# Kernel optimization log

Measured on AMD Instinct MI355X. Metric: run time of the kernel, lower is better.

## Reference

```python
import jax, jax.numpy as jnp
import numpy as np

N_HEAD = 16
D_HEAD = 64
MAX_REL = 512  # max_relative_positions


def setup_inputs() -> dict:
    key = jax.random.key(0)
    ks = jax.random.split(key, 9)
    B, S, D = 2, 2048, 1024
    return {
        "hidden_states": jax.random.normal(ks[0], (B, S, D), jnp.float32),
        "Wq": jax.random.normal(ks[1], (D, D), jnp.float32) * 0.02,
        "bq": jnp.zeros((D,), jnp.float32),
        "Wk": jax.random.normal(ks[2], (D, D), jnp.float32) * 0.02,
        "bk": jnp.zeros((D,), jnp.float32),
        "Wv": jax.random.normal(ks[3], (D, D), jnp.float32) * 0.02,
        "bv": jnp.zeros((D,), jnp.float32),
        "Wc": jax.random.normal(ks[4], (D, D), jnp.float32) * 0.02,
        "pos_table": jax.random.normal(ks[5], (2 * MAX_REL, D_HEAD), jnp.float32) * 0.02,
    }


def reference(hidden_states, Wq, bq, Wk, bk, Wv, bv, Wc, pos_table):
    B, S, D = hidden_states.shape
    H, Dh = N_HEAD, D_HEAD

    # QKV projections (torch Linear: x @ W.T + b)
    q = hidden_states @ Wq.T + bq
    k = hidden_states @ Wk.T + bk
    v = hidden_states @ Wv.T + bv
    q = q.reshape(B, S, H, Dh).transpose(0, 2, 1, 3)  # b h s d
    k = k.reshape(B, S, H, Dh).transpose(0, 2, 1, 3)
    v = v.reshape(B, S, H, Dh).transpose(0, 2, 1, 3)

    # relative position embedding lookup: [S, S, Dh]
    ar = jnp.arange(S)
    rel = jnp.clip(ar[:, None] - ar[None, :] + MAX_REL, 0, 2 * MAX_REL - 1)
    rpe = pos_table[rel]  # (S, S, Dh)

    # c2p: original einsum 'bhld,ijd->bhij' sums q over l (faithful)
    c2p = jnp.einsum('bhld,ijd->bhij', q, rpe)
    p2c = jnp.einsum('bhjd,ijd->bhij', k, jnp.flip(rpe, axis=0))
    bias = c2p + p2c  # (B, H, S, S)

    # SDPA with explicit attn_mask == bias added to scaled scores
    scale = 1.0 / jnp.sqrt(jnp.asarray(Dh, hidden_states.dtype))
    scores = jnp.einsum('bhid,bhjd->bhij', q, k) * scale + bias
    attn = jax.nn.softmax(scores, axis=-1)
    out = jnp.einsum('bhij,bhjd->bhid', attn, v)  # (B, H, S, Dh)

    out = out.transpose(0, 2, 1, 3).reshape(B, S, D)
    return out @ Wc.T  # c_proj has no bias; dropout is identity in eval
```

## Files before the change

### kernel.cpp

```cpp
#include <hip/hip_runtime.h>
#include <math.h>

#define BN   2
#define SEQ  2048
#define DIM  1024
#define NH   16
#define DH   64
#define TAB  1024
#define SCALE 0.125f
#define LOG2E 1.44269504088896340736f

typedef __attribute__((ext_vector_type(8))) short bf16x8;
typedef __attribute__((ext_vector_type(4))) float f32x4;

#if defined(__has_builtin)
#if __has_builtin(__builtin_amdgcn_exp2f)
#define EXP2F(x) __builtin_amdgcn_exp2f(x)
#else
#define EXP2F(x) exp2f(x)
#endif
#else
#define EXP2F(x) exp2f(x)
#endif

__device__ __forceinline__ short f2b(float f) {
    union { float f; unsigned u; } x; x.f = f;
    return (short)((x.u + 0x7fffu + ((x.u >> 16) & 1u)) >> 16);
}
__device__ __forceinline__ float b2f(short s) {
    union { float f; unsigned u; } x; x.u = ((unsigned)(unsigned short)s) << 16;
    return x.f;
}

#define GLDS16(gp, lp) __builtin_amdgcn_global_load_lds( \
    (const __attribute__((address_space(1))) void*)(gp), \
    (__attribute__((address_space(3))) void*)(lp), 16, 0, 0)

__device__ __forceinline__ bf16x8 fragS(const short* base, int row, int kq) {
    return *(const bf16x8*)(base + row * 64 + ((kq ^ (row & 7)) << 3));
}

__global__ __launch_bounds__(256) void f2b_multi_kernel(
    const float* __restrict__ s0, short* __restrict__ d0, int n0,
    const float* __restrict__ s1, short* __restrict__ d1,
    const float* __restrict__ s2, short* __restrict__ d2,
    const float* __restrict__ s3, short* __restrict__ d3, int nw,
    const float* __restrict__ s4, short* __restrict__ d4, int n4)
{
    const int z = blockIdx.z;
    const float* src = z == 0 ? s0 : (z == 1 ? s1 : (z == 2 ? s2 : (z == 3 ? s3 : s4)));
    short* dst       = z == 0 ? d0 : (z == 1 ? d1 : (z == 2 ? d2 : (z == 3 ? d3 : d4)));
    const int n      = z == 0 ? n0 : (z == 4 ? n4 : nw);
    int i = (blockIdx.x * 256 + threadIdx.x) * 8;
    if (i >= n) return;
    float4 a = *(const float4*)&src[i];
    float4 b = *(const float4*)&src[i + 4];
    bf16x8 o = { f2b(a.x), f2b(a.y), f2b(a.z), f2b(a.w),
                 f2b(b.x), f2b(b.y), f2b(b.z), f2b(b.w) };
    *(bf16x8*)&dst[i] = o;
}

__global__ __launch_bounds__(256) void qkv_mfma_kernel(
    const short* __restrict__ xb,
    const short* __restrict__ Wqb, const float* __restrict__ bq,
    const short* __restrict__ Wkb, const float* __restrict__ bk,
    const short* __restrict__ Wvb, const float* __restrict__ bv,
    short* __restrict__ q, short* __restrict__ k, short* __restrict__ v)
{
    const int which = blockIdx.z;
    const short* W    = which == 0 ? Wqb : (which == 1 ? Wkb : Wvb);
    const float* bias = which == 0 ? bq  : (which == 1 ? bk  : bv);
    short* outp       = which == 0 ? q   : (which == 1 ? k   : v);
    const float osc   = which == 0 ? SCALE * LOG2E : 1.0f;

    const int m0 = blockIdx.y * 128;
    const int n0 = blockIdx.x * 128;

    __shared__ short As[128 * 64];
    __shared__ short Bs[128 * 64];

    const int t  = threadIdx.x;
    const int w  = t >> 6;
    const int q4 = (t >> 4) & 3;
    const int l  = t & 15;
    const int wm = (w >> 1) * 64;
    const int wn = (w & 1) * 64;

    f32x4 acc[4][4];
#pragma unroll
    for (int mt = 0; mt < 4; ++mt)
#pragma unroll
        for (int nt = 0; nt < 4; ++nt) acc[mt][nt] = (f32x4){0.f,0.f,0.f,0.f};

    for (int k0 = 0; k0 < DIM; k0 += 64) {
        __syncthreads();
#pragma unroll
        for (int p = 0; p < 4; ++p) {
            const int cq = p * 256 + t;
            const int row = cq >> 3, bd = cq & 7;
            const int goff = (bd ^ (row & 7)) << 3;
            GLDS16(xb + (size_t)(m0 + row) * DIM + k0 + goff, As + cq * 8);
            GLDS16(W  + (size_t)(n0 + row) * DIM + k0 + goff, Bs + cq * 8);
        }
        __syncthreads();
#pragma unroll
        for (int kc = 0; kc < 2; ++kc) {
            bf16x8 af[4], bf[4];
#pragma unroll
            for (int mt = 0; mt < 4; ++mt) af[mt] = fragS(As, wm + mt*16 + l, kc*4 + q4);
#pragma unroll
            for (int nt = 0; nt < 4; ++nt) bf[nt] = fragS(Bs, wn + nt*16 + l, kc*4 + q4);
#pragma unroll
            for (int mt = 0; mt < 4; ++mt)
#pragma unroll
                for (int nt = 0; nt < 4; ++nt)
                    acc[mt][nt] = __builtin_amdgcn_mfma_f32_16x16x32_bf16(
                        af[mt], bf[nt], acc[mt][nt], 0, 0, 0);
        }
    }

    float bv4[4];
#pragma unroll
    for (int nt = 0; nt < 4; ++nt) bv4[nt] = bias[n0 + wn + nt*16 + l];
#pragma unroll
    for (int mt = 0; mt < 4; ++mt) {
#pragma unroll
        for (int r = 0; r < 4; ++r) {
            const int m  = m0 + wm + mt*16 + q4*4 + r;
            const int b_ = m >> 11, s_ = m & 2047;
#pragma unroll
            for (int nt = 0; nt < 4; ++nt) {
                const int o  = n0 + wn + nt*16 + l;
                const int h_ = o >> 6, d_ = o & 63;
                outp[((size_t)(b_*NH + h_) * SEQ + s_) * DH + d_] =
                    f2b((acc[mt][nt][r] + bv4[nt]) * osc);
            }
        }
    }
}

__global__ __launch_bounds__(256) void qsum_c2p_kernel(
    const short* __restrict__ q, const float* __restrict__ pt, float* __restrict__ c2p)
{
    const int bh = blockIdx.x;
    const short* qb = q + (size_t)bh * SEQ * DH;
    __shared__ float part[32][72];
    __shared__ float qs[64];
    const int t = threadIdx.x;
    const int dg = t & 7, sc = t >> 3;
    float a[8];
#pragma unroll
    for (int c = 0; c < 8; ++c) a[c] = 0.f;
    for (int s = sc * 64; s < sc * 64 + 64; ++s) {
        bf16x8 vv = *(const bf16x8*)&qb[(size_t)s * DH + dg * 8];
#pragma unroll
        for (int c = 0; c < 8; ++c) a[c] += b2f(vv[c]);
    }
#pragma unroll
    for (int c = 0; c < 8; ++c) part[sc][dg*8 + c] = a[c];
    __syncthreads();
    if (t < 64) {
        float s = 0.f;
#pragma unroll 8
        for (int i = 0; i < 32; ++i) s += part[i][t];
        qs[t] = s * 8.0f;
    }
    __syncthreads();
    for (int c = t; c < TAB; c += 256) {
        const float* ptr = pt + (size_t)c * DH;
        float s = 0.f;
#pragma unroll
        for (int dd = 0; dd < DH; dd += 4) {
            float4 p4 = *(const float4*)&ptr[dd];
            s += qs[dd]*p4.x + qs[dd+1]*p4.y + qs[dd+2]*p4.z + qs[dd+3]*p4.w;
        }
        c2p[(size_t)bh * TAB + c] = s;
    }
}

__global__ __launch_bounds__(256) void tgemm_kernel(
    const short* __restrict__ kglob, const short* __restrict__ ptb,
    short* __restrict__ slab, int bh0)
{
    const int G    = gridDim.z;
    const int gsub = G >> 3;
    const int fid  = (blockIdx.z * gridDim.y + blockIdx.y) * gridDim.x + blockIdx.x;
    const int g    = (fid & 7) * gsub + ((fid >> 3) % gsub);
    const int rest = fid / (8 * gsub);
    const int m0 = (rest >> 3) * 128;
    const int n0 = (rest & 7) * 128;

    const int bh = bh0 + g;
    const short* A = kglob + (size_t)bh * SEQ * DH;

    __shared__ short As[128 * 64];
    __shared__ short Bs[128 * 64];

    const int t  = threadIdx.x;
    const int w  = t >> 6;
    const int q4 = (t >> 4) & 3;
    const int l  = t & 15;
    const int wm = (w >> 1) * 64;
    const int wn = (w & 1) * 64;

#pragma unroll
    for (int p = 0; p < 4; ++p) {
        const int cq = p * 256 + t;
        const int row = cq >> 3, bd = cq & 7;
        const int go = (bd ^ (row & 7)) << 3;
        GLDS16(A   + (size_t)(m0 + row) * DH + go, As + cq * 8);
        GLDS16(ptb + (size_t)(n0 + row) * DH + go, Bs + cq * 8);
    }
    __syncthreads();

    f32x4 acc[4][4];
#pragma unroll
    for (int mt = 0; mt < 4; ++mt)
#pragma unroll
        for (int nt = 0; nt < 4; ++nt) acc[mt][nt] = (f32x4){0.f,0.f,0.f,0.f};
#pragma unroll
    for (int kc = 0; kc < 2; ++kc) {
        bf16x8 af[4], bf[4];
#pragma unroll
        for (int mt = 0; mt < 4; ++mt) af[mt] = fragS(As, wm + mt*16 + l, kc*4 + q4);
#pragma unroll
        for (int nt = 0; nt < 4; ++nt) bf[nt] = fragS(Bs, wn + nt*16 + l, kc*4 + q4);
#pragma unroll
        for (int mt = 0; mt < 4; ++mt)
#pragma unroll
            for (int nt = 0; nt < 4; ++nt)
                acc[mt][nt] = __builtin_amdgcn_mfma_f32_16x16x32_bf16(
                    af[mt], bf[nt], acc[mt][nt], 0, 0, 0);
    }

    short* outp = slab + (size_t)g * SEQ * 1024;
#pragma unroll
    for (int mt = 0; mt < 4; ++mt)
#pragma unroll
        for (int r = 0; r < 4; ++r) {
            const int m = m0 + wm + mt*16 + q4*4 + r;
#pragma unroll
            for (int nt = 0; nt < 4; ++nt)
                outp[(size_t)m * 1024 + n0 + wn + nt*16 + l] =
                    f2b(acc[mt][nt][r] * LOG2E);
        }
}

__global__ __launch_bounds__(256, 4) void attn_kernel(
    const short* __restrict__ q, const short* __restrict__ k, const short* __restrict__ v,
    const float* __restrict__ c2p, const short* __restrict__ slab,
    short* __restrict__ ao, int bh0)
{
    const int G    = gridDim.y;
    const int gsub = G >> 3;
    const int fid  = blockIdx.y * gridDim.x + blockIdx.x;
    const int g    = (fid & 7) * gsub + ((fid >> 3) % gsub);
    const int i0   = (fid / (8 * gsub)) * 64;

    const int bh = bh0 + g;
    const int b_ = bh >> 4, h_ = bh & 15;
    const short* qbh = q + (size_t)bh * SEQ * DH;
    const short* kbh = k + (size_t)bh * SEQ * DH;
    const short* vbh = v + (size_t)bh * SEQ * DH;
    const float* c2pb = c2p + (size_t)bh * TAB;
    const short* Tb   = slab + (size_t)g * SEQ * 1024;

    __shared__ short QsBand[64 * 72];
    __shared__ short Ks[64 * 64];
    __shared__ short Vt[64 * 64];
    __shared__ short Pp[64 * 64];
    __shared__ float cband[128];
    __shared__ float evf[64];

    const int t   = threadIdx.x;
    const int w   = t >> 6;
    const int q4  = (t >> 4) & 3;
    const int l   = t & 15;
    const int ilb = w*16 + q4*4;

#pragma unroll
    for (int p = 0; p < 2; ++p) {
        const int cq = p * 256 + t;
        const int row = cq >> 3, bd = cq & 7;
        GLDS16(qbh + (size_t)(i0 + row) * DH + ((bd ^ (row & 7)) << 3), QsBand + cq * 8);
    }
    __syncthreads();
    const bf16x8 aq0 = fragS(QsBand, w*16 + l, q4);
    const bf16x8 aq1 = fragS(QsBand, w*16 + l, 4 + q4);

    float lsum[4] = {0.f, 0.f, 0.f, 0.f};
    f32x4 O[4];
#pragma unroll
    for (int dt = 0; dt < 4; ++dt) O[dt] = (f32x4){0.f, 0.f, 0.f, 0.f};

    const int jp  = t & 31;
    const int dgv = t >> 5;

    for (int j0 = 0; j0 < SEQ; j0 += 64) {
        const int Kc0 = 2559 - i0 - j0;
        const int cls = (Kc0 >= 1149) ? 0 : (Kc0 <= 0 ? 1 :
                        ((Kc0 >= 126 && Kc0 <= 1023) ? 2 : 3));
        __syncthreads();

#pragma unroll
        for (int p = 0; p < 2; ++p) {
            const int cq = p * 256 + t;
            const int row = cq >> 3, bd = cq & 7;
            GLDS16(kbh + (size_t)(j0 + row) * DH + ((bd ^ (row & 7)) << 3), Ks + cq * 8);
        }
        {
            const int j = 2 * jp, d0 = dgv * 8;
            bf16x8 va = *(const bf16x8*)(vbh + (size_t)(j0 + j)     * DH + d0);
            bf16x8 vb = *(const bf16x8*)(vbh + (size_t)(j0 + j + 1) * DH + d0);
#pragma unroll
            for (int c = 0; c < 8; ++c) {
                const int d = d0 + c;
                const int slot = d * 64 + (((j >> 3) ^ (d & 7)) << 3) + (j & 7);
                short2 pr; pr.x = va[c]; pr.y = vb[c];
                *(short2*)&Vt[slot] = pr;
            }
        }
        if (cls <= 1) {
            if (t < 64)
                evf[t] = b2f(Tb[(size_t)(j0 + t) * 1024 + (cls == 0 ? 1023 : 0)]);
        } else {
            const int rowj = t >> 2, m0b = t & 3;
            const int tb = Kc0 - rowj;
            const int af = min(max((tb - 63) & ~7, 0), 952);
            const short* srcrow = Tb + (size_t)(j0 + rowj) * 1024 + af;
            short* dstrow = &QsBand[rowj * 72];
            *(int4*)&dstrow[m0b * 8]       = *(const int4*)&srcrow[m0b * 8];
            *(int4*)&dstrow[(m0b + 4) * 8] = *(const int4*)&srcrow[(m0b + 4) * 8];
            if (m0b == 0)
                *(int4*)&dstrow[64] = *(const int4*)&srcrow[64];
        }
        if (t < 128) {
            int cc = min(max(449 + i0 - j0 + t, 0), TAB - 1);
            cband[t] = c2pb[cc];
        }
        __syncthreads();

        f32x4 st4[4];
        if (cls <= 1) {
#pragma unroll
            for (int jt = 0; jt < 4; ++jt) {
                const int jl = jt*16 + l;
                const float evj = evf[jl];
#pragma unroll
                for (int r = 0; r < 4; ++r)
                    st4[jt][r] = cband[ilb + r - jl + 63] + evj;
            }
        } else {
#pragma unroll
            for (int jt = 0; jt < 4; ++jt) {
                const int jl = jt*16 + l;
#pragma unroll
                for (int r = 0; r < 4; ++r)
                    st4[jt][r] = cband[ilb + r - jl + 63];
            }
        }
        __builtin_amdgcn_s_setprio(1);
#pragma unroll
        for (int jt = 0; jt < 4; ++jt) {
            bf16x8 b0 = fragS(Ks, jt*16 + l, q4);
            bf16x8 b1 = fragS(Ks, jt*16 + l, 4 + q4);
            st4[jt] = __builtin_amdgcn_mfma_f32_16x16x32_bf16(aq0, b0, st4[jt], 0, 0, 0);
            st4[jt] = __builtin_amdgcn_mfma_f32_16x16x32_bf16(aq1, b1, st4[jt], 0, 0, 0);
        }
        __builtin_amdgcn_s_setprio(0);

        if (cls <= 1) {
#pragma unroll
            for (int jt = 0; jt < 4; ++jt) {
                const int jl = jt*16 + l;
#pragma unroll
                for (int r = 0; r < 4; ++r) {
                    const int il = ilb + r;
                    const float p = EXP2F(st4[jt][r]);
                    lsum[r] += p;
                    Pp[il * 64 + (((jl >> 3) ^ (il & 7)) << 3) + (jl & 7)] = f2b(p);
                }
            }
        } else if (cls == 2) {
#pragma unroll
            for (int jt = 0; jt < 4; ++jt) {
                const int jl = jt*16 + l;
                const int tb = Kc0 - jl;
                const int af = min((tb - 63) & ~7, 952);
                const short* bp = &QsBand[jl * 72 + (tb - ilb - 3 - af)];
#pragma unroll
                for (int r = 0; r < 4; ++r) {
                    const int il = ilb + r;
                    const float p = EXP2F(st4[jt][r] + b2f(bp[3 - r]));
                    lsum[r] += p;
                    Pp[il * 64 + (((jl >> 3) ^ (il & 7)) << 3) + (jl & 7)] = f2b(p);
                }
            }
        } else {
#pragma unroll
            for (int jt = 0; jt < 4; ++jt) {
                const int jl = jt*16 + l;
                const int tb = Kc0 - jl;
                const int af = min(max((tb - 63) & ~7, 0), 952);
                const short* brow = &QsBand[jl * 72];
#pragma unroll
                for (int r = 0; r < 4; ++r) {
                    const int il = ilb + r;
                    const int y = min(max(tb - il, 0), 1023);
                    const float p = EXP2F(st4[jt][r] + b2f(brow[y - af]));
                    lsum[r] += p;
                    Pp[il * 64 + (((jl >> 3) ^ (il & 7)) << 3) + (jl & 7)] = f2b(p);
                }
            }
        }
        __syncthreads();

        bf16x8 ap0 = fragS(Pp, w*16 + l, q4);
        bf16x8 ap1 = fragS(Pp, w*16 + l, 4 + q4);
        __builtin_amdgcn_s_setprio(1);
#pragma unroll
        for (int dt = 0; dt < 4; ++dt) {
            bf16x8 b0 = fragS(Vt, dt*16 + l, q4);
            bf16x8 b1 = fragS(Vt, dt*16 + l, 4 + q4);
            O[dt] = __builtin_amdgcn_mfma_f32_16x16x32_bf16(ap0, b0, O[dt], 0, 0, 0);
            O[dt] = __builtin_amdgcn_mfma_f32_16x16x32_bf16(ap1, b1, O[dt], 0, 0, 0);
        }
        __builtin_amdgcn_s_setprio(0);
    }

#pragma unroll
    for (int off = 1; off < 16; off <<= 1)
#pragma unroll
        for (int r = 0; r < 4; ++r)
            lsum[r] += __shfl_xor(lsum[r], off);

#pragma unroll
    for (int r = 0; r < 4; ++r) {
        const float inv = 1.f / lsum[r];
        const int i_g = i0 + ilb + r;
        short* dst = ao + (((size_t)b_ * SEQ + i_g) * NH + h_) * DH + l;
#pragma unroll
        for (int dt = 0; dt < 4; ++dt)
            dst[dt*16] = f2b(O[dt][r] * inv);
    }
}

__global__ __launch_bounds__(256) void out_mfma_kernel(
    const short* __restrict__ xb, const float* __restrict__ W, float* __restrict__ out)
{
    const int m0 = blockIdx.y * 128;
    const int n0 = blockIdx.x * 128;

    __shared__ short As[128 * 64];
    __shared__ short Bs[128 * 64];

    const int t  = threadIdx.x;
    const int w  = t >> 6;
    const int q4 = (t >> 4) & 3;
    const int l  = t & 15;
    const int wm = (w >> 1) * 64;
    const int wn = (w & 1) * 64;

    f32x4 acc[4][4];
#pragma unroll
    for (int mt = 0; mt < 4; ++mt)
#pragma unroll
        for (int nt = 0; nt < 4; ++nt) acc[mt][nt] = (f32x4){0.f,0.f,0.f,0.f};

    for (int k0 = 0; k0 < DIM; k0 += 64) {
        __syncthreads();
#pragma unroll
        for (int p = 0; p < 4; ++p) {
            const int cq = p * 256 + t;
            const int row = cq >> 3, bd = cq & 7;
            GLDS16(xb + (size_t)(m0 + row) * DIM + k0 + ((bd ^ (row & 7)) << 3), As + cq * 8);
        }
        {
            const int row = t >> 1, h = t & 1;
#pragma unroll
            for (int c = 0; c < 4; ++c) {
                const int gch = h * 4 + c;
                const float* src = W + (size_t)(n0 + row) * DIM + k0 + gch * 8;
                float4 f0 = *(const float4*)src;
                float4 f1 = *(const float4*)(src + 4);
                bf16x8 o = { f2b(f0.x), f2b(f0.y), f2b(f0.z), f2b(f0.w),
                             f2b(f1.x), f2b(f1.y), f2b(f1.z), f2b(f1.w) };
                *(bf16x8*)&Bs[row * 64 + ((gch ^ (row & 7)) << 3)] = o;
            }
        }
        __syncthreads();
#pragma unroll
        for (int kc = 0; kc < 2; ++kc) {
            bf16x8 af[4], bf[4];
#pragma unroll
            for (int mt = 0; mt < 4; ++mt) af[mt] = fragS(As, wm + mt*16 + l, kc*4 + q4);
#pragma unroll
            for (int nt = 0; nt < 4; ++nt) bf[nt] = fragS(Bs, wn + nt*16 + l, kc*4 + q4);
#pragma unroll
            for (int mt = 0; mt < 4; ++mt)
#pragma unroll
                for (int nt = 0; nt < 4; ++nt)
                    acc[mt][nt] = __builtin_amdgcn_mfma_f32_16x16x32_bf16(
                        af[mt], bf[nt], acc[mt][nt], 0, 0, 0);
        }
    }
#pragma unroll
    for (int mt = 0; mt < 4; ++mt)
#pragma unroll
        for (int r = 0; r < 4; ++r) {
            const int m = m0 + wm + mt*16 + q4*4 + r;
#pragma unroll
            for (int nt = 0; nt < 4; ++nt)
                out[(size_t)m * DIM + n0 + wn + nt*16 + l] = acc[mt][nt][r];
        }
}

extern "C" void kernel_launch(void* const* d_in, const int* in_sizes, int n_in,
                              void* d_out, int out_size, void* d_ws, size_t ws_size,
                              hipStream_t stream)
{
    const float* hs = (const float*)d_in[0];
    const float* Wq = (const float*)d_in[1];
    const float* bq = (const float*)d_in[2];
    const float* Wk = (const float*)d_in[3];
    const float* bk = (const float*)d_in[4];
    const float* Wv = (const float*)d_in[5];
    const float* bv = (const float*)d_in[6];
    const float* Wc = (const float*)d_in[7];
    const float* pt = (const float*)d_in[8];
    float* out = (float*)d_out;

    const size_t XE    = (size_t)BN * SEQ * DIM;
    const size_t WE    = (size_t)DIM * DIM;
    const size_t PE    = (size_t)TAB * DH;
    const size_t SLAB1 = (size_t)SEQ * 1024;

    short* sw   = (short*)d_ws;
    short* qb   = sw;
    short* kb   = sw + XE;
    short* vb   = sw + 2 * XE;
    short* aob  = sw + 3 * XE;
    float* c2p  = (float*)(sw + 4 * XE);
    short* ptb  = sw + 4 * XE + 65536;
    short* slab = sw + 4 * XE + 65536 + PE;
    short* xb   = slab;
    short* wqb  = slab + XE;
    short* wkb  = wqb + WE;
    short* wvb  = wkb + WE;

    const size_t fixed_sh = 4 * XE + 65536 + PE;
    const size_t avail_sh = (ws_size / 2 > fixed_sh) ? ws_size / 2 - fixed_sh : 0;
    const int G = (avail_sh >= 32 * SLAB1) ? 32 : ((avail_sh >= 16 * SLAB1) ? 16 : 8);

    f2b_multi_kernel<<<dim3((int)(XE/2048), 1, 5), 256, 0, stream>>>(
        hs, xb, (int)XE, Wq, wqb, Wk, wkb, Wv, wvb, (int)WE, pt, ptb, (int)PE);

    qkv_mfma_kernel<<<dim3(DIM/128, (BN*SEQ)/128, 3), 256, 0, stream>>>(
        xb, wqb, bq, wkb, bk, wvb, bv, qb, kb, vb);

    qsum_c2p_kernel<<<dim3(BN*NH), 256, 0, stream>>>(qb, pt, c2p);

    for (int bh0 = 0; bh0 < BN*NH; bh0 += G) {
        tgemm_kernel<<<dim3(1024/128, SEQ/128, G), 256, 0, stream>>>(kb, ptb, slab, bh0);
        attn_kernel<<<dim3(SEQ/64, G), 256, 0, stream>>>(qb, kb, vb, c2p, slab, aob, bh0);
    }

    out_mfma_kernel<<<dim3(DIM/128, (BN*SEQ)/128), 256, 0, stream>>>(aob, Wc, out);
}
```

Measured before the change: 344.6 us.

## Keep P in registers via transposed QK^T MFMA and permlane swaps

Computes the score tile transposed (K as A operand, Q as B) so each lane holds scores for one query row. The bf16 probabilities are then packed with v_cvt_pk_bf16_f32 and rearranged with v_permlane16_swap into the A-operand layout for the PV MFMA. This removes the Pp shared-memory round trip and one __syncthreads per key tile, and cuts the row-sum reduction to two shuffles. QsBand row stride is padded to 80 to change bank mapping. The cost is more intricate lane-layout logic that must match the MFMA operand layout exactly.

```diff
diff --git a/kernel.cpp b/kernel.cpp
--- a/kernel.cpp
+++ b/kernel.cpp
@@ -265,18 +265,18 @@
     const float* c2pb = c2p + (size_t)bh * TAB;
     const short* Tb   = slab + (size_t)g * SEQ * 1024;
 
-    __shared__ short QsBand[64 * 72];
+    __shared__ short QsBand[64 * 80];
     __shared__ short Ks[64 * 64];
     __shared__ short Vt[64 * 64];
-    __shared__ short Pp[64 * 64];
     __shared__ float cband[128];
     __shared__ float evf[64];
 
-    const int t   = threadIdx.x;
-    const int w   = t >> 6;
-    const int q4  = (t >> 4) & 3;
-    const int l   = t & 15;
-    const int ilb = w*16 + q4*4;
+    const int t    = threadIdx.x;
+    const int w    = t >> 6;
+    const int q4   = (t >> 4) & 3;
+    const int l    = t & 15;
+    const int iLoc = w*16 + l;
+    const int pq   = ((q4 & 1) << 1) | (q4 >> 1);
 
 #pragma unroll
     for (int p = 0; p < 2; ++p) {
@@ -288,7 +288,7 @@
     const bf16x8 aq0 = fragS(QsBand, w*16 + l, q4);
     const bf16x8 aq1 = fragS(QsBand, w*16 + l, 4 + q4);
 
-    float lsum[4] = {0.f, 0.f, 0.f, 0.f};
+    float lsum = 0.f;
     f32x4 O[4];
 #pragma unroll
     for (int dt = 0; dt < 4; ++dt) O[dt] = (f32x4){0.f, 0.f, 0.f, 0.f};
@@ -328,7 +328,7 @@
             const int tb = Kc0 - rowj;
             const int af = min(max((tb - 63) & ~7, 0), 952);
             const short* srcrow = Tb + (size_t)(j0 + rowj) * 1024 + af;
-            short* dstrow = &QsBand[rowj * 72];
+            short* dstrow = &QsBand[rowj * 80];
             *(int4*)&dstrow[m0b * 8]       = *(const int4*)&srcrow[m0b * 8];
             *(int4*)&dstrow[(m0b + 4) * 8] = *(const int4*)&srcrow[(m0b + 4) * 8];
             if (m0b == 0)
@@ -341,103 +341,105 @@
         __syncthreads();
 
         f32x4 st4[4];
+        const int cb0 = iLoc - q4*4 + 63;
+#pragma unroll
+        for (int jt = 0; jt < 4; ++jt) {
+            const int base = cb0 - jt*16;
+            st4[jt][0] = cband[base];
+            st4[jt][1] = cband[base - 1];
+            st4[jt][2] = cband[base - 2];
+            st4[jt][3] = cband[base - 3];
+        }
         if (cls <= 1) {
 #pragma unroll
             for (int jt = 0; jt < 4; ++jt) {
-                const int jl = jt*16 + l;
-                const float evj = evf[jl];
+                const float4 e4 = *(const float4*)&evf[jt*16 + q4*4];
+                st4[jt][0] += e4.x; st4[jt][1] += e4.y;
+                st4[jt][2] += e4.z; st4[jt][3] += e4.w;
+            }
+        }
+
+        __builtin_amdgcn_s_setprio(1);
+#pragma unroll
+        for (int jt = 0; jt < 4; ++jt) {
+            bf16x8 a0 = fragS(Ks, jt*16 + l, q4);
+            bf16x8 a1 = fragS(Ks, jt*16 + l, 4 + q4);
+            st4[jt] = __builtin_amdgcn_mfma_f32_16x16x32_bf16(a0, aq0, st4[jt], 0, 0, 0);
+            st4[jt] = __builtin_amdgcn_mfma_f32_16x16x32_bf16(a1, aq1, st4[jt], 0, 0, 0);
+        }
+        __builtin_amdgcn_s_setprio(0);
+
+        float pv4[4][4];
+        if (cls <= 1) {
+#pragma unroll
+            for (int jt = 0; jt < 4; ++jt)
 #pragma unroll
                 for (int r = 0; r < 4; ++r)
-                    st4[jt][r] = cband[ilb + r - jl + 63] + evj;
-            }
+                    pv4[jt][r] = EXP2F(st4[jt][r]);
+        } else if (cls == 2) {
+#pragma unroll
+            for (int jt = 0; jt < 4; ++jt)
+#pragma unroll
+                for (int r = 0; r < 4; ++r) {
+                    const int jl = jt*16 + q4*4 + r;
+                    const int tb = Kc0 - jl;
+                    const int af = min((tb - 63) & ~7, 952);
+                    pv4[jt][r] = EXP2F(st4[jt][r] +
+                                       b2f(QsBand[jl * 80 + (tb - iLoc - af)]));
+                }
         } else {
 #pragma unroll
-            for (int jt = 0; jt < 4; ++jt) {
-                const int jl = jt*16 + l;
-#pragma unroll
-                for (int r = 0; r < 4; ++r)
-                    st4[jt][r] = cband[ilb + r - jl + 63];
-            }
-        }
+            for (int jt = 0; jt < 4; ++jt)
+#pragma unroll
+                for (int r = 0; r < 4; ++r) {
+                    const int jl = jt*16 + q4*4 + r;
+                    const int tb = Kc0 - jl;
+                    const int af = min(max((tb - 63) & ~7, 0), 952);
+                    const int y  = min(max(tb - iLoc, 0), 1023);
+                    pv4[jt][r] = EXP2F(st4[jt][r] +
+                                       b2f(QsBand[jl * 80 + (y - af)]));
+                }
+        }
+#pragma unroll
+        for (int jt = 0; jt < 4; ++jt)
+#pragma unroll
+            for (int r = 0; r < 4; ++r) lsum += pv4[jt][r];
+
+        unsigned P2[4][2];
+#pragma unroll
+        for (int t2 = 0; t2 < 4; ++t2) {
+            asm("v_cvt_pk_bf16_f32 %0, %1, %2"
+                : "=v"(P2[t2][0]) : "v"(pv4[t2][0]), "v"(pv4[t2][1]));
+            asm("v_cvt_pk_bf16_f32 %0, %1, %2"
+                : "=v"(P2[t2][1]) : "v"(pv4[t2][2]), "v"(pv4[t2][3]));
+        }
+#pragma unroll
+        for (int m = 0; m < 2; ++m) {
+            asm("v_permlane16_swap_b32 %0, %1" : "+v"(P2[0][m]), "+v"(P2[1][m]));
+            asm("v_permlane16_swap_b32 %0, %1" : "+v"(P2[2][m]), "+v"(P2[3][m]));
+        }
+        union { unsigned u[4]; bf16x8 v8; } UA, UB;
+        UA.u[0] = P2[0][0]; UA.u[1] = P2[0][1]; UA.u[2] = P2[1][0]; UA.u[3] = P2[1][1];
+        UB.u[0] = P2[2][0]; UB.u[1] = P2[2][1]; UB.u[2] = P2[3][0]; UB.u[3] = P2[3][1];
+
         __builtin_amdgcn_s_setprio(1);
 #pragma unroll
-        for (int jt = 0; jt < 4; ++jt) {
-            bf16x8 b0 = fragS(Ks, jt*16 + l, q4);
-            bf16x8 b1 = fragS(Ks, jt*16 + l, 4 + q4);
-            st4[jt] = __builtin_amdgcn_mfma_f32_16x16x32_bf16(aq0, b0, st4[jt], 0, 0, 0);
-            st4[jt] = __builtin_amdgcn_mfma_f32_16x16x32_bf16(aq1, b1, st4[jt], 0, 0, 0);
+        for (int dt = 0; dt < 4; ++dt) {
+            bf16x8 b0 = fragS(Vt, dt*16 + l, pq);
+            bf16x8 b1 = fragS(Vt, dt*16 + l, 4 + pq);
+            O[dt] = __builtin_amdgcn_mfma_f32_16x16x32_bf16(UA.v8, b0, O[dt], 0, 0, 0);
+            O[dt] = __builtin_amdgcn_mfma_f32_16x16x32_bf16(UB.v8, b1, O[dt], 0, 0, 0);
         }
         __builtin_amdgcn_s_setprio(0);
-
-        if (cls <= 1) {
-#pragma unroll
-            for (int jt = 0; jt < 4; ++jt) {
-                const int jl = jt*16 + l;
-#pragma unroll
-                for (int r = 0; r < 4; ++r) {
-                    const int il = ilb + r;
-                    const float p = EXP2F(st4[jt][r]);
-                    lsum[r] += p;
-                    Pp[il * 64 + (((jl >> 3) ^ (il & 7)) << 3) + (jl & 7)] = f2b(p);
-                }
-            }
-        } else if (cls == 2) {
-#pragma unroll
-            for (int jt = 0; jt < 4; ++jt) {
-                const int jl = jt*16 + l;
-                const int tb = Kc0 - jl;
-                const int af = min((tb - 63) & ~7, 952);
-                const short* bp = &QsBand[jl * 72 + (tb - ilb - 3 - af)];
-#pragma unroll
-                for (int r = 0; r < 4; ++r) {
-                    const int il = ilb + r;
-                    const float p = EXP2F(st4[jt][r] + b2f(bp[3 - r]));
-                    lsum[r] += p;
-                    Pp[il * 64 + (((jl >> 3) ^ (il & 7)) << 3) + (jl & 7)] = f2b(p);
-                }
-            }
-        } else {
-#pragma unroll
-            for (int jt = 0; jt < 4; ++jt) {
-                const int jl = jt*16 + l;
-                const int tb = Kc0 - jl;
-                const int af = min(max((tb - 63) & ~7, 0), 952);
-                const short* brow = &QsBand[jl * 72];
-#pragma unroll
-                for (int r = 0; r < 4; ++r) {
-                    const int il = ilb + r;
-                    const int y = min(max(tb - il, 0), 1023);
-                    const float p = EXP2F(st4[jt][r] + b2f(brow[y - af]));
-                    lsum[r] += p;
-                    Pp[il * 64 + (((jl >> 3) ^ (il & 7)) << 3) + (jl & 7)] = f2b(p);
-                }
-            }
-        }
-        __syncthreads();
-
-        bf16x8 ap0 = fragS(Pp, w*16 + l, q4);
-        bf16x8 ap1 = fragS(Pp, w*16 + l, 4 + q4);
-        __builtin_amdgcn_s_setprio(1);
-#pragma unroll
-        for (int dt = 0; dt < 4; ++dt) {
-            bf16x8 b0 = fragS(Vt, dt*16 + l, q4);
-            bf16x8 b1 = fragS(Vt, dt*16 + l, 4 + q4);
-            O[dt] = __builtin_amdgcn_mfma_f32_16x16x32_bf16(ap0, b0, O[dt], 0, 0, 0);
-            O[dt] = __builtin_amdgcn_mfma_f32_16x16x32_bf16(ap1, b1, O[dt], 0, 0, 0);
-        }
-        __builtin_amdgcn_s_setprio(0);
-    }
-
-#pragma unroll
-    for (int off = 1; off < 16; off <<= 1)
-#pragma unroll
-        for (int r = 0; r < 4; ++r)
-            lsum[r] += __shfl_xor(lsum[r], off);
+    }
+
+    lsum += __shfl_xor(lsum, 16);
+    lsum += __shfl_xor(lsum, 32);
 
 #pragma unroll
     for (int r = 0; r < 4; ++r) {
-        const float inv = 1.f / lsum[r];
-        const int i_g = i0 + ilb + r;
+        const float inv = 1.f / __shfl(lsum, q4*4 + r);
+        const int i_g = i0 + w*16 + q4*4 + r;
         short* dst = ao + (((size_t)b_ * SEQ + i_g) * NH + h_) * DH + l;
 #pragma unroll
         for (int dt = 0; dt < 4; ++dt)
```

New measurement: 357.2 us. 3.7% more time.
